# Optimization experiments

Hardware: AMD Instinct MI355X
Metric: run time of the kernel (lower is better)

## Reference

```python
import jax, jax.numpy as jnp
import numpy as np


def setup_inputs() -> dict:
    key = jax.random.key(0)
    ks = jax.random.split(key, 8)
    B, T, H, Hu = 128, 64, 1024, 512
    MJW = 64                    # max_jump_width
    J = 2 * MJW + 1             # size_jump_width_set_nn = 129
    N = 2 * T                   # HMM states (word states + null states)
    I = 64                      # source sentence length
    sc = 0.02
    return {
        "y_hidden": jax.random.normal(ks[0], (B, T, H), jnp.float32),
        # emission probs p(source word i | state s), strictly positive for log
        "emission": jax.random.uniform(ks[1], (B, N, I), jnp.float32, 1e-4, 1.0),
        "source_lengths": jax.random.randint(ks[2], (B,), 1, I + 1),
        "W1": jax.random.normal(ks[3], (H, Hu), jnp.float32) * sc,
        "b1": jnp.zeros((Hu,), jnp.float32),
        "W2": jax.random.normal(ks[4], (Hu, J), jnp.float32) * sc,
        "b2": jnp.zeros((J,), jnp.float32),
        "W3": jax.random.normal(ks[5], (Hu, 1), jnp.float32) * sc,
        "b3": jnp.zeros((1,), jnp.float32),
        "max_jump_width": MJW,
    }


def _build_transition(y_hidden, W1, b1, W2, b2, W3, b3, mjw):
    # Dense(tanh) -> Dense softmax jump-width distribution + Dense sigmoid p0
    B, T, _ = y_hidden.shape
    ts = jnp.tanh(y_hidden @ W1 + b1)                       # [B,T,Hu]
    jw = jax.nn.softmax(ts @ W2 + b2, axis=-1)              # [B,T,J]
    p0 = jax.nn.sigmoid(jnp.squeeze(ts @ W3 + b3, -1))      # [B,T]
    r = jnp.arange(T)
    # banded gather: transition[i, j] = jw[i, mjw + j - i]
    band_idx = mjw + r[None, :] - r[:, None]                # [T,T], in [0, J)
    band = jnp.take_along_axis(jw, band_idx[None], axis=2)  # [B,T,T]
    diag_p0 = jnp.eye(T, dtype=jw.dtype) * p0[:, :, None]   # [B,T,T]
    top = jnp.concatenate([band, diag_p0], axis=2)          # [B,T,2T]
    return jnp.concatenate([top, top], axis=1)              # [B,2T,2T]


def _forward_alignment(transition, emission, source_lengths):
    # Faithful translation of the tf.scan forward algorithm. tf.scan with no
    # initializer uses elems[0] as the initial accumulator and emits it as
    # output[0] (log part = ones, so the [0,0] element is 1.0).
    B, N, I = emission.shape
    em = jnp.transpose(emission, (2, 0, 1))                 # [I,B,N]
    alpha0 = jnp.broadcast_to(em[0][:, None, :], (B, N, N)) # rows all equal e_0
    L0 = jnp.ones((B,), emission.dtype)

    def step(carry, e):
        alpha, L = carry                                    # [B,N,N], [B]
        yi = e[:, None, :]                                  # rows of yi_prob identical
        m1 = jnp.matmul(alpha, transition)                  # [B,N,N]
        tmp = m1 * yi
        tmp = tmp / jnp.sum(tmp, axis=2, keepdims=True)     # row-normalized alpha
        m2 = jnp.matmul(transition, alpha) * yi             # [B,N,N]
        max_j = jnp.max(m2, axis=-1)[:, 0]                  # gather row 0 -> [B]
        state_prev = jnp.sum(m1, axis=1)                    # [B,N]
        state = jnp.log(e) + jnp.log(state_prev) - max_j[:, None]
        state_log = jnp.log(jnp.sum(jnp.exp(state), axis=-1))
        L_new = L + state_log + max_j                       # [B]
        return (tmp, L_new), L_new

    (_, _), logs = jax.lax.scan(step, (alpha0, L0), em[1:])  # [I-1,B]
    logs = jnp.concatenate([L0[None], logs], axis=0).T       # [B,I]
    idx = (source_lengths - 1)[:, None]
    return jnp.take_along_axis(logs, idx, axis=1)[:, 0]      # [B]


def reference(y_hidden, emission, source_lengths, W1, b1, W2, b2, W3, b3, max_jump_width):
    transition = _build_transition(y_hidden, W1, b1, W2, b2, W3, b3, max_jump_width)
    return _forward_alignment(transition, emission, source_lengths)
```

## Files before the change

### kernel.cpp

```cpp
#include <hip/hip_runtime.h>
#include <hip/hip_bf16.h>

typedef float f32x4 __attribute__((ext_vector_type(4)));
typedef __bf16 bf16x8 __attribute__((ext_vector_type(8)));
typedef unsigned short u16;

#define OFF_W1T  0u
#define OFF_W23B 1048576u
#define OFF_TS   1196032u
#define OFF_JWS  9584640u
#define OFF_P0   11681792u

static __device__ __forceinline__ u16 f2bf(float x) {
    __bf16 h = (__bf16)x;
    return __builtin_bit_cast(u16, h);
}

__global__ __launch_bounds__(256) void prep_kernel(
    const float* __restrict__ W1, const float* __restrict__ W2,
    const float* __restrict__ W3,
    __bf16* __restrict__ W1T, __bf16* __restrict__ W23B)
{
    const int t = threadIdx.x;
    if (blockIdx.x < 128) {
        __shared__ __bf16 lds_t[64][72];
        const int kt = blockIdx.x >> 3, nt = blockIdx.x & 7;
        const int k0 = kt * 64, n0 = nt * 64;
        {
            const int kr = t >> 2, c0 = (t & 3) * 16;
            const float* src = W1 + (size_t)(k0 + kr) * 512 + n0 + c0;
            #pragma unroll
            for (int q = 0; q < 4; ++q) {
                float4 v = *(const float4*)(src + q * 4);
                lds_t[kr][c0 + q * 4 + 0] = (__bf16)v.x;
                lds_t[kr][c0 + q * 4 + 1] = (__bf16)v.y;
                lds_t[kr][c0 + q * 4 + 2] = (__bf16)v.z;
                lds_t[kr][c0 + q * 4 + 3] = (__bf16)v.w;
            }
        }
        __syncthreads();
        {
            const int nr = t >> 2, kc = (t & 3) * 16;
            bf16x8 o0, o1;
            #pragma unroll
            for (int j = 0; j < 8; ++j) o0[j] = lds_t[kc + j][nr];
            #pragma unroll
            for (int j = 0; j < 8; ++j) o1[j] = lds_t[kc + 8 + j][nr];
            __bf16* dst = W1T + (size_t)(n0 + nr) * 1024 + k0 + kc;
            *(bf16x8*)(dst)     = o0;
            *(bf16x8*)(dst + 8) = o1;
        }
    } else {
        int g = (blockIdx.x - 128) * 256 + t;
        if (g < 9216) {
            int n = g >> 6;
            int k8 = (g & 63) * 8;
            bf16x8 v;
            #pragma unroll
            for (int j = 0; j < 8; ++j) {
                int k = k8 + j;
                float x = 0.0f;
                if (n < 129) x = W2[(size_t)k * 129 + n];
                else if (n == 129) x = W3[k];
                v[j] = (__bf16)x;
            }
            int kk = k8 >> 5, lg = (k8 >> 3) & 3, ct = n >> 4, lr = n & 15;
            W23B[(((size_t)(kk * 9 + ct)) * 64 + lg * 16 + lr) * 8] = v[0];
            *(bf16x8*)&W23B[(((size_t)(kk * 9 + ct)) * 64 + lg * 16 + lr) * 8] = v;
        }
    }
}

struct Stage {
    float4 a0, a1, a2, a3;
    uint4  b0, b1;
};

__global__ __launch_bounds__(512) void gemm1_kernel(
    const float* __restrict__ Y, const __bf16* __restrict__ W1T,
    const float* __restrict__ b1, u16* __restrict__ ts)
{
    __shared__ __bf16 As[2][128 * 64];
    __shared__ __bf16 Bs[2][128 * 64];
    const int tid = threadIdx.x;
    const int m0 = blockIdx.x * 128, n0 = blockIdx.y * 128;
    const int wid = tid >> 6, lane = tid & 63;
    const int wr = wid >> 2, wc = wid & 3;
    const int lr = lane & 15, lg = lane >> 4;

    const int ra = tid >> 2;
    const int kc = (tid & 3) * 16;
    const int esw = ((ra & 7) << 3);
    const int e0 = kc ^ esw;
    const int e1 = (kc + 8) ^ esw;

    const float*  ya = Y   + (size_t)(m0 + ra) * 1024 + kc;
    const __bf16* wb = W1T + (size_t)(n0 + ra) * 1024 + kc;

    f32x4 acc[4][2];
    #pragma unroll
    for (int m = 0; m < 4; m++)
        #pragma unroll
        for (int n = 0; n < 2; n++) { f32x4 z = {0.f,0.f,0.f,0.f}; acc[m][n] = z; }

#define ISSUE(S, kt) do { \
    const float4* yp = (const float4*)(ya + (kt) * 64); \
    (S).a0 = yp[0]; (S).a1 = yp[1]; (S).a2 = yp[2]; (S).a3 = yp[3]; \
    const uint4* wp = (const uint4*)(wb + (kt) * 64); \
    (S).b0 = wp[0]; (S).b1 = wp[1]; \
} while (0)

#define WRITE(S, buf) do { \
    bf16x8 pa0, pa1; \
    pa0[0]=(__bf16)(S).a0.x; pa0[1]=(__bf16)(S).a0.y; pa0[2]=(__bf16)(S).a0.z; pa0[3]=(__bf16)(S).a0.w; \
    pa0[4]=(__bf16)(S).a1.x; pa0[5]=(__bf16)(S).a1.y; pa0[6]=(__bf16)(S).a1.z; pa0[7]=(__bf16)(S).a1.w; \
    pa1[0]=(__bf16)(S).a2.x; pa1[1]=(__bf16)(S).a2.y; pa1[2]=(__bf16)(S).a2.z; pa1[3]=(__bf16)(S).a2.w; \
    pa1[4]=(__bf16)(S).a3.x; pa1[5]=(__bf16)(S).a3.y; pa1[6]=(__bf16)(S).a3.z; pa1[7]=(__bf16)(S).a3.w; \
    *(bf16x8*)&As[buf][ra * 64 + e0] = pa0; \
    *(bf16x8*)&As[buf][ra * 64 + e1] = pa1; \
    *(uint4*)&Bs[buf][ra * 64 + e0] = (S).b0; \
    *(uint4*)&Bs[buf][ra * 64 + e1] = (S).b1; \
} while (0)

#define BARRIER() do { \
    asm volatile("s_waitcnt lgkmcnt(0)" ::: "memory"); \
    __builtin_amdgcn_s_barrier(); \
} while (0)

#define COMPUTE(buf) do { \
    const int swl = (lr & 7) << 3; \
    _Pragma("unroll") \
    for (int ks = 0; ks < 2; ++ks) { \
        const int eoff = (ks * 32 + lg * 8) ^ swl; \
        bf16x8 af[4], bfr[2]; \
        _Pragma("unroll") \
        for (int m = 0; m < 4; ++m) af[m] = *(const bf16x8*)&As[buf][(wr * 64 + m * 16 + lr) * 64 + eoff]; \
        _Pragma("unroll") \
        for (int n = 0; n < 2; ++n) bfr[n] = *(const bf16x8*)&Bs[buf][(wc * 32 + n * 16 + lr) * 64 + eoff]; \
        __builtin_amdgcn_s_setprio(1); \
        _Pragma("unroll") \
        for (int m = 0; m < 4; ++m) \
            _Pragma("unroll") \
            for (int n = 0; n < 2; ++n) \
                acc[m][n] = __builtin_amdgcn_mfma_f32_16x16x32_bf16(af[m], bfr[n], acc[m][n], 0, 0, 0); \
        __builtin_amdgcn_s_setprio(0); \
    } \
} while (0)

    Stage SA, SB;
    ISSUE(SA, 0);
    #pragma unroll 1
    for (int kt = 0; kt < 16; kt += 2) {
        ISSUE(SB, kt + 1);
        WRITE(SA, 0);
        BARRIER();
        COMPUTE(0);
        if (kt + 2 < 16) ISSUE(SA, kt + 2);
        WRITE(SB, 1);
        BARRIER();
        COMPUTE(1);
    }

    #pragma unroll
    for (int m = 0; m < 4; m++) {
        #pragma unroll
        for (int n = 0; n < 2; n++) {
            int col = n0 + wc * 32 + n * 16 + lr;
            float bias = b1[col];
            #pragma unroll
            for (int j = 0; j < 4; j++) {
                int row = m0 + wr * 64 + m * 16 + lg * 4 + j;
                float v = tanhf(acc[m][n][j] + bias);
                ts[(size_t)row * 512 + col] = f2bf(v);
            }
        }
    }
#undef ISSUE
#undef WRITE
#undef BARRIER
#undef COMPUTE
}

__global__ __launch_bounds__(128) void gemm2_kernel(
    const u16* __restrict__ ts, const u16* __restrict__ W23B,
    const float* __restrict__ b2, const float* __restrict__ b3,
    float* __restrict__ jwS, float* __restrict__ p0)
{
    const int tid = threadIdx.x;
    const int lane = tid & 63, w = tid >> 6;
    const int r0 = blockIdx.x * 32 + w * 16;
    const int lr = lane & 15, lg = lane >> 4;

    f32x4 acc[9];
    #pragma unroll
    for (int ct = 0; ct < 9; ct++) { f32x4 z = {0.f,0.f,0.f,0.f}; acc[ct] = z; }

    #pragma unroll 4
    for (int kk = 0; kk < 16; ++kk) {
        bf16x8 a = *(const bf16x8*)(ts + (size_t)(r0 + lr) * 512 + kk * 32 + lg * 8);
        #pragma unroll
        for (int ct = 0; ct < 9; ct++) {
            bf16x8 bv = *(const bf16x8*)(W23B + ((size_t)(kk * 9 + ct) * 64 + lane) * 8);
            acc[ct] = __builtin_amdgcn_mfma_f32_16x16x32_bf16(a, bv, acc[ct], 0, 0, 0);
        }
    }

    float b3v = b3[0];
    #pragma unroll
    for (int j = 0; j < 4; j++) {
        int row = r0 + lg * 4 + j;
        int trow = row & 63;
        float v[9];
        float mx = -1e30f;
        #pragma unroll
        for (int ct = 0; ct < 9; ct++) {
            int col = ct * 16 + lr;
            if (col < 129) { float x = acc[ct][j] + b2[col]; v[ct] = x; mx = fmaxf(mx, x); }
            else v[ct] = -1e30f;
        }
        #pragma unroll
        for (int o = 1; o < 16; o <<= 1) mx = fmaxf(mx, __shfl_xor(mx, o));
        float sum = 0.f;
        #pragma unroll
        for (int ct = 0; ct < 9; ct++) {
            int col = ct * 16 + lr;
            if (col < 129) { float e = expf(v[ct] - mx); v[ct] = e; sum += e; }
        }
        #pragma unroll
        for (int o = 1; o < 16; o <<= 1) sum += __shfl_xor(sum, o);
        float inv = 1.0f / sum;
        #pragma unroll
        for (int ct = 0; ct < 9; ct++) {
            int col = ct * 16 + lr;
            int cc = col - 64 + trow;
            if (col < 129 && cc >= 0 && cc < 64)
                jwS[(size_t)row * 64 + cc] = v[ct] * inv;
        }
        if (lr == 1) {
            float pv = acc[8][j] + b3v;
            p0[row] = 1.0f / (1.0f + expf(-pv));
        }
    }
}

__global__ __launch_bounds__(64) void recur_kernel(
    const float* __restrict__ jwS, const float* __restrict__ p0g,
    const float* __restrict__ em, const int* __restrict__ slen,
    float* __restrict__ out)
{
    __shared__ float em_s[128][65];
    __shared__ float atil_s[64];
    const int b = blockIdx.x, c = threadIdx.x;

    float breg[64];
    const float* jwb = jwS + (size_t)b * 64 * 64;
    #pragma unroll
    for (int it = 0; it < 64; ++it) breg[it] = jwb[it * 64 + c];

    const float4* eg = (const float4*)(em + (size_t)b * 8192);
    #pragma unroll 4
    for (int i4 = c; i4 < 2048; i4 += 64) {
        float4 v = eg[i4];
        int base = i4 * 4; int n = base >> 6; int ii = base & 63;
        em_s[n][ii] = v.x; em_s[n][ii + 1] = v.y; em_s[n][ii + 2] = v.z; em_s[n][ii + 3] = v.w;
    }
    float p0r = p0g[b * 64 + c];
    const int idx = slen[b] - 1;
    __syncthreads();

    float atil = em_s[c][0] + em_s[c + 64][0];
    atil_s[c] = atil;
    float Lacc = 0.f;
    __syncthreads();

    for (int i = 1; i <= idx; ++i) {
        float s0 = 0.f, s1 = 0.f, s2 = 0.f, s3 = 0.f;
        #pragma unroll
        for (int it4 = 0; it4 < 16; ++it4) {
            float4 av = *(const float4*)&atil_s[it4 * 4];
            s0 = fmaf(av.x, breg[it4 * 4 + 0], s0);
            s1 = fmaf(av.y, breg[it4 * 4 + 1], s1);
            s2 = fmaf(av.z, breg[it4 * 4 + 2], s2);
            s3 = fmaf(av.w, breg[it4 * 4 + 3], s3);
        }
        float ut = ((s0 + s1) + (s2 + s3)) * em_s[c][i]
                 + atil * p0r * em_s[c + 64][i];
        if (((i & 3) == 0) || (i == idx)) {
            float r = ut;
            #pragma unroll
            for (int o = 1; o < 64; o <<= 1) r += __shfl_xor(r, o);
            Lacc += __log2f(r);
            ut *= __builtin_amdgcn_rcpf(r);
        }
        atil = ut;
        atil_s[c] = ut;
        __syncthreads();
    }
    if (c == 0) out[b] = 1.0f + 0.6931471805599453f * (Lacc + 7.0f * (float)idx);
}

extern "C" void kernel_launch(void* const* d_in, const int* in_sizes, int n_in,
                              void* d_out, int out_size, void* d_ws, size_t ws_size,
                              hipStream_t stream)
{
    const float* Y   = (const float*)d_in[0];
    const float* em  = (const float*)d_in[1];
    const int*   sl  = (const int*)d_in[2];
    const float* W1  = (const float*)d_in[3];
    const float* b1  = (const float*)d_in[4];
    const float* W2  = (const float*)d_in[5];
    const float* b2  = (const float*)d_in[6];
    const float* W3  = (const float*)d_in[7];
    const float* b3  = (const float*)d_in[8];
    float* out = (float*)d_out;
    char* ws = (char*)d_ws;

    __bf16* W1T  = (__bf16*)(ws + OFF_W1T);
    __bf16* W23B = (__bf16*)(ws + OFF_W23B);
    u16*    ts   = (u16*)(ws + OFF_TS);
    float*  jwS  = (float*)(ws + OFF_JWS);
    float*  p0   = (float*)(ws + OFF_P0);

    prep_kernel<<<164, 256, 0, stream>>>(W1, W2, W3, W1T, W23B);
    dim3 g1(64, 4);
    gemm1_kernel<<<g1, 512, 0, stream>>>(Y, W1T, b1, ts);
    gemm2_kernel<<<256, 128, 0, stream>>>(ts, (const u16*)W23B, b2, b3, jwS, p0);
    recur_kernel<<<128, 64, 0, stream>>>(jwS, p0, em, sl, out);
}
```

Measured before the change: 86.54 us.

## Fuse gemm2 with recurrence, use readlane broadcast, retile gemm1 to 64-row blocks

Merges the jump-width softmax GEMM and the forward recurrence into one kernel per batch. The banded transition and p0 now stay in shared memory instead of going through a global round trip. The recurrence now broadcasts alpha across lanes with readlane instead of writing to LDS and calling __syncthreads every step. gemm1 is retiled to 64x128 blocks of 256 threads, giving 512 blocks for better CU occupancy. The trade-off is that only one wave per batch runs the serial recurrence, and gemm2 now has only 128 blocks.

```diff
diff --git a/kernel.cpp b/kernel.cpp
--- a/kernel.cpp
+++ b/kernel.cpp
@@ -8,13 +8,13 @@
 #define OFF_W1T  0u
 #define OFF_W23B 1048576u
 #define OFF_TS   1196032u
-#define OFF_JWS  9584640u
-#define OFF_P0   11681792u
 
 static __device__ __forceinline__ u16 f2bf(float x) {
     __bf16 h = (__bf16)x;
     return __builtin_bit_cast(u16, h);
 }
+
+#define RL(x, l) __int_as_float(__builtin_amdgcn_readlane(__float_as_int(x), (l)))
 
 __global__ __launch_bounds__(256) void prep_kernel(
     const float* __restrict__ W1, const float* __restrict__ W2,
@@ -65,37 +65,35 @@
                 v[j] = (__bf16)x;
             }
             int kk = k8 >> 5, lg = (k8 >> 3) & 3, ct = n >> 4, lr = n & 15;
-            W23B[(((size_t)(kk * 9 + ct)) * 64 + lg * 16 + lr) * 8] = v[0];
             *(bf16x8*)&W23B[(((size_t)(kk * 9 + ct)) * 64 + lg * 16 + lr) * 8] = v;
         }
     }
 }
 
-struct Stage {
-    float4 a0, a1, a2, a3;
-    uint4  b0, b1;
-};
-
-__global__ __launch_bounds__(512) void gemm1_kernel(
+struct StageA { float4 a0, a1, a2, a3; };
+struct StageB { uint4 b0, b1, b2, b3; };
+
+__global__ __launch_bounds__(256, 2) void gemm1_kernel(
     const float* __restrict__ Y, const __bf16* __restrict__ W1T,
     const float* __restrict__ b1, u16* __restrict__ ts)
 {
-    __shared__ __bf16 As[2][128 * 64];
+    __shared__ __bf16 As[2][64 * 64];
     __shared__ __bf16 Bs[2][128 * 64];
     const int tid = threadIdx.x;
-    const int m0 = blockIdx.x * 128, n0 = blockIdx.y * 128;
+    const int m0 = blockIdx.x * 64, n0 = blockIdx.y * 128;
     const int wid = tid >> 6, lane = tid & 63;
-    const int wr = wid >> 2, wc = wid & 3;
     const int lr = lane & 15, lg = lane >> 4;
 
-    const int ra = tid >> 2;
-    const int kc = (tid & 3) * 16;
-    const int esw = ((ra & 7) << 3);
-    const int e0 = kc ^ esw;
-    const int e1 = (kc + 8) ^ esw;
-
-    const float*  ya = Y   + (size_t)(m0 + ra) * 1024 + kc;
-    const __bf16* wb = W1T + (size_t)(n0 + ra) * 1024 + kc;
+    const int ar = tid >> 2, akc = (tid & 3) * 16;
+    const int asw = (ar & 7) << 3;
+    const int ae0 = akc ^ asw, ae1 = (akc + 8) ^ asw;
+    const int br = tid >> 1, bkc = (tid & 1) * 32;
+    const int bsw = (br & 7) << 3;
+    const int be0 = bkc ^ bsw, be1 = (bkc + 8) ^ bsw;
+    const int be2 = (bkc + 16) ^ bsw, be3 = (bkc + 24) ^ bsw;
+
+    const float*  ya = Y   + (size_t)(m0 + ar) * 1024 + akc;
+    const __bf16* wb = W1T + (size_t)(n0 + br) * 1024 + bkc;
 
     f32x4 acc[4][2];
     #pragma unroll
@@ -103,23 +101,25 @@
         #pragma unroll
         for (int n = 0; n < 2; n++) { f32x4 z = {0.f,0.f,0.f,0.f}; acc[m][n] = z; }
 
-#define ISSUE(S, kt) do { \
+#define ISSUE(SA_, SB_, kt) do { \
     const float4* yp = (const float4*)(ya + (kt) * 64); \
-    (S).a0 = yp[0]; (S).a1 = yp[1]; (S).a2 = yp[2]; (S).a3 = yp[3]; \
+    (SA_).a0 = yp[0]; (SA_).a1 = yp[1]; (SA_).a2 = yp[2]; (SA_).a3 = yp[3]; \
     const uint4* wp = (const uint4*)(wb + (kt) * 64); \
-    (S).b0 = wp[0]; (S).b1 = wp[1]; \
+    (SB_).b0 = wp[0]; (SB_).b1 = wp[1]; (SB_).b2 = wp[2]; (SB_).b3 = wp[3]; \
 } while (0)
 
-#define WRITE(S, buf) do { \
+#define WRITE(SA_, SB_, buf) do { \
     bf16x8 pa0, pa1; \
-    pa0[0]=(__bf16)(S).a0.x; pa0[1]=(__bf16)(S).a0.y; pa0[2]=(__bf16)(S).a0.z; pa0[3]=(__bf16)(S).a0.w; \
-    pa0[4]=(__bf16)(S).a1.x; pa0[5]=(__bf16)(S).a1.y; pa0[6]=(__bf16)(S).a1.z; pa0[7]=(__bf16)(S).a1.w; \
-    pa1[0]=(__bf16)(S).a2.x; pa1[1]=(__bf16)(S).a2.y; pa1[2]=(__bf16)(S).a2.z; pa1[3]=(__bf16)(S).a2.w; \
-    pa1[4]=(__bf16)(S).a3.x; pa1[5]=(__bf16)(S).a3.y; pa1[6]=(__bf16)(S).a3.z; pa1[7]=(__bf16)(S).a3.w; \
-    *(bf16x8*)&As[buf][ra * 64 + e0] = pa0; \
-    *(bf16x8*)&As[buf][ra * 64 + e1] = pa1; \
-    *(uint4*)&Bs[buf][ra * 64 + e0] = (S).b0; \
-    *(uint4*)&Bs[buf][ra * 64 + e1] = (S).b1; \
+    pa0[0]=(__bf16)(SA_).a0.x; pa0[1]=(__bf16)(SA_).a0.y; pa0[2]=(__bf16)(SA_).a0.z; pa0[3]=(__bf16)(SA_).a0.w; \
+    pa0[4]=(__bf16)(SA_).a1.x; pa0[5]=(__bf16)(SA_).a1.y; pa0[6]=(__bf16)(SA_).a1.z; pa0[7]=(__bf16)(SA_).a1.w; \
+    pa1[0]=(__bf16)(SA_).a2.x; pa1[1]=(__bf16)(SA_).a2.y; pa1[2]=(__bf16)(SA_).a2.z; pa1[3]=(__bf16)(SA_).a2.w; \
+    pa1[4]=(__bf16)(SA_).a3.x; pa1[5]=(__bf16)(SA_).a3.y; pa1[6]=(__bf16)(SA_).a3.z; pa1[7]=(__bf16)(SA_).a3.w; \
+    *(bf16x8*)&As[buf][ar * 64 + ae0] = pa0; \
+    *(bf16x8*)&As[buf][ar * 64 + ae1] = pa1; \
+    *(uint4*)&Bs[buf][br * 64 + be0] = (SB_).b0; \
+    *(uint4*)&Bs[buf][br * 64 + be1] = (SB_).b1; \
+    *(uint4*)&Bs[buf][br * 64 + be2] = (SB_).b2; \
+    *(uint4*)&Bs[buf][br * 64 + be3] = (SB_).b3; \
 } while (0)
 
 #define BARRIER() do { \
@@ -134,9 +134,9 @@
         const int eoff = (ks * 32 + lg * 8) ^ swl; \
         bf16x8 af[4], bfr[2]; \
         _Pragma("unroll") \
-        for (int m = 0; m < 4; ++m) af[m] = *(const bf16x8*)&As[buf][(wr * 64 + m * 16 + lr) * 64 + eoff]; \
+        for (int m = 0; m < 4; ++m) af[m] = *(const bf16x8*)&As[buf][(m * 16 + lr) * 64 + eoff]; \
         _Pragma("unroll") \
-        for (int n = 0; n < 2; ++n) bfr[n] = *(const bf16x8*)&Bs[buf][(wc * 32 + n * 16 + lr) * 64 + eoff]; \
+        for (int n = 0; n < 2; ++n) bfr[n] = *(const bf16x8*)&Bs[buf][(wid * 32 + n * 16 + lr) * 64 + eoff]; \
         __builtin_amdgcn_s_setprio(1); \
         _Pragma("unroll") \
         for (int m = 0; m < 4; ++m) \
@@ -147,16 +147,16 @@
     } \
 } while (0)
 
-    Stage SA, SB;
-    ISSUE(SA, 0);
+    StageA A0, A1; StageB B0, B1;
+    ISSUE(A0, B0, 0);
     #pragma unroll 1
     for (int kt = 0; kt < 16; kt += 2) {
-        ISSUE(SB, kt + 1);
-        WRITE(SA, 0);
+        ISSUE(A1, B1, kt + 1);
+        WRITE(A0, B0, 0);
         BARRIER();
         COMPUTE(0);
-        if (kt + 2 < 16) ISSUE(SA, kt + 2);
-        WRITE(SB, 1);
+        if (kt + 2 < 16) ISSUE(A0, B0, kt + 2);
+        WRITE(A1, B1, 1);
         BARRIER();
         COMPUTE(1);
     }
@@ -165,11 +165,11 @@
     for (int m = 0; m < 4; m++) {
         #pragma unroll
         for (int n = 0; n < 2; n++) {
-            int col = n0 + wc * 32 + n * 16 + lr;
+            int col = n0 + wid * 32 + n * 16 + lr;
             float bias = b1[col];
             #pragma unroll
             for (int j = 0; j < 4; j++) {
-                int row = m0 + wr * 64 + m * 16 + lg * 4 + j;
+                int row = m0 + m * 16 + lg * 4 + j;
                 float v = tanhf(acc[m][n][j] + bias);
                 ts[(size_t)row * 512 + col] = f2bf(v);
             }
@@ -181,15 +181,31 @@
 #undef COMPUTE
 }
 
-__global__ __launch_bounds__(128) void gemm2_kernel(
+__global__ __launch_bounds__(256) void gemm2_recur_kernel(
     const u16* __restrict__ ts, const u16* __restrict__ W23B,
     const float* __restrict__ b2, const float* __restrict__ b3,
-    float* __restrict__ jwS, float* __restrict__ p0)
+    const float* __restrict__ em, const int* __restrict__ slen,
+    float* __restrict__ out)
 {
+    __shared__ float jw_s[64][65];
+    __shared__ float em_s[128][65];
+    __shared__ float p0_s[64];
+    const int b = blockIdx.x;
     const int tid = threadIdx.x;
-    const int lane = tid & 63, w = tid >> 6;
-    const int r0 = blockIdx.x * 32 + w * 16;
+    const int w = tid >> 6, lane = tid & 63;
     const int lr = lane & 15, lg = lane >> 4;
+    const int r0 = b * 64 + w * 16;
+
+    {
+        const float4* eg = (const float4*)(em + (size_t)b * 8192);
+        #pragma unroll
+        for (int q = 0; q < 8; ++q) {
+            int i4 = tid + q * 256;
+            float4 v = eg[i4];
+            int base = i4 * 4; int n = base >> 6; int ii = base & 63;
+            em_s[n][ii] = v.x; em_s[n][ii + 1] = v.y; em_s[n][ii + 2] = v.z; em_s[n][ii + 3] = v.w;
+        }
+    }
 
     f32x4 acc[9];
     #pragma unroll
@@ -208,8 +224,7 @@
     float b3v = b3[0];
     #pragma unroll
     for (int j = 0; j < 4; j++) {
-        int row = r0 + lg * 4 + j;
-        int trow = row & 63;
+        int rloc = w * 16 + lg * 4 + j;
         float v[9];
         float mx = -1e30f;
         #pragma unroll
@@ -232,59 +247,41 @@
         #pragma unroll
         for (int ct = 0; ct < 9; ct++) {
             int col = ct * 16 + lr;
-            int cc = col - 64 + trow;
+            int cc = col - 64 + rloc;
             if (col < 129 && cc >= 0 && cc < 64)
-                jwS[(size_t)row * 64 + cc] = v[ct] * inv;
+                jw_s[rloc][cc] = v[ct] * inv;
         }
         if (lr == 1) {
             float pv = acc[8][j] + b3v;
-            p0[row] = 1.0f / (1.0f + expf(-pv));
-        }
-    }
-}
-
-__global__ __launch_bounds__(64) void recur_kernel(
-    const float* __restrict__ jwS, const float* __restrict__ p0g,
-    const float* __restrict__ em, const int* __restrict__ slen,
-    float* __restrict__ out)
-{
-    __shared__ float em_s[128][65];
-    __shared__ float atil_s[64];
-    const int b = blockIdx.x, c = threadIdx.x;
-
+            p0_s[rloc] = 1.0f / (1.0f + expf(-pv));
+        }
+    }
+    __syncthreads();
+    if (tid >= 64) return;
+
+    const int c = tid;
     float breg[64];
-    const float* jwb = jwS + (size_t)b * 64 * 64;
-    #pragma unroll
-    for (int it = 0; it < 64; ++it) breg[it] = jwb[it * 64 + c];
-
-    const float4* eg = (const float4*)(em + (size_t)b * 8192);
-    #pragma unroll 4
-    for (int i4 = c; i4 < 2048; i4 += 64) {
-        float4 v = eg[i4];
-        int base = i4 * 4; int n = base >> 6; int ii = base & 63;
-        em_s[n][ii] = v.x; em_s[n][ii + 1] = v.y; em_s[n][ii + 2] = v.z; em_s[n][ii + 3] = v.w;
-    }
-    float p0r = p0g[b * 64 + c];
+    #pragma unroll
+    for (int it = 0; it < 64; ++it) breg[it] = jw_s[it][c];
+    const float p0r = p0_s[c];
     const int idx = slen[b] - 1;
-    __syncthreads();
 
     float atil = em_s[c][0] + em_s[c + 64][0];
-    atil_s[c] = atil;
     float Lacc = 0.f;
-    __syncthreads();
-
+
+    #pragma unroll 1
     for (int i = 1; i <= idx; ++i) {
+        float em_lo = em_s[c][i];
+        float em_hi = em_s[c + 64][i];
         float s0 = 0.f, s1 = 0.f, s2 = 0.f, s3 = 0.f;
         #pragma unroll
-        for (int it4 = 0; it4 < 16; ++it4) {
-            float4 av = *(const float4*)&atil_s[it4 * 4];
-            s0 = fmaf(av.x, breg[it4 * 4 + 0], s0);
-            s1 = fmaf(av.y, breg[it4 * 4 + 1], s1);
-            s2 = fmaf(av.z, breg[it4 * 4 + 2], s2);
-            s3 = fmaf(av.w, breg[it4 * 4 + 3], s3);
-        }
-        float ut = ((s0 + s1) + (s2 + s3)) * em_s[c][i]
-                 + atil * p0r * em_s[c + 64][i];
+        for (int k = 0; k < 16; ++k) {
+            s0 = fmaf(RL(atil, 4 * k + 0), breg[4 * k + 0], s0);
+            s1 = fmaf(RL(atil, 4 * k + 1), breg[4 * k + 1], s1);
+            s2 = fmaf(RL(atil, 4 * k + 2), breg[4 * k + 2], s2);
+            s3 = fmaf(RL(atil, 4 * k + 3), breg[4 * k + 3], s3);
+        }
+        float ut = ((s0 + s1) + (s2 + s3)) * em_lo + atil * p0r * em_hi;
         if (((i & 3) == 0) || (i == idx)) {
             float r = ut;
             #pragma unroll
@@ -293,8 +290,6 @@
             ut *= __builtin_amdgcn_rcpf(r);
         }
         atil = ut;
-        atil_s[c] = ut;
-        __syncthreads();
     }
     if (c == 0) out[b] = 1.0f + 0.6931471805599453f * (Lacc + 7.0f * (float)idx);
 }
@@ -318,12 +313,9 @@
     __bf16* W1T  = (__bf16*)(ws + OFF_W1T);
     __bf16* W23B = (__bf16*)(ws + OFF_W23B);
     u16*    ts   = (u16*)(ws + OFF_TS);
-    float*  jwS  = (float*)(ws + OFF_JWS);
-    float*  p0   = (float*)(ws + OFF_P0);
 
     prep_kernel<<<164, 256, 0, stream>>>(W1, W2, W3, W1T, W23B);
-    dim3 g1(64, 4);
-    gemm1_kernel<<<g1, 512, 0, stream>>>(Y, W1T, b1, ts);
-    gemm2_kernel<<<256, 128, 0, stream>>>(ts, (const u16*)W23B, b2, b3, jwS, p0);
-    recur_kernel<<<128, 64, 0, stream>>>(jwS, p0, em, sl, out);
-}
+    dim3 g1(128, 4);
+    gemm1_kernel<<<g1, 256, 0, stream>>>(Y, W1T, b1, ts);
+    gemm2_recur_kernel<<<128, 256, 0, stream>>>(ts, (const u16*)W23B, b2, b3, em, sl, out);
+}
```

Measured after the change: 91.72 us. 6.0% more time.
